# Optimization experiments

Hardware: AMD Instinct MI355X
Metric: run time of the kernel (lower is better)

Reference implementation:

```python
import jax, jax.numpy as jnp
import numpy as np
import jax.lax as lax

B, S, E, H = 8, 4096, 1024, 128
TAU = 1.0
MIN_K = 32

def setup_inputs() -> dict:
    key = jax.random.key(0)
    k0, k1, k2, k3 = jax.random.split(key, 4)
    token_embeddings = jax.random.normal(k0, (B, S, E), dtype=jnp.float32)
    w1 = jax.random.normal(k1, (E, H), dtype=jnp.float32) * (1.0 / np.sqrt(E))
    b1 = jnp.zeros((H,), dtype=jnp.float32)
    w2 = jax.random.normal(k2, (H, 1), dtype=jnp.float32) * (1.0 / np.sqrt(H))
    b2 = jnp.zeros((1,), dtype=jnp.float32)
    # uniform noise for Gumbel, same bounds as the original module
    u = jax.random.uniform(k3, (B, S), minval=1e-08, maxval=1.0 - 1e-08, dtype=jnp.float32)
    return {"token_embeddings": token_embeddings, "w1": w1, "b1": b1, "w2": w2, "b2": b2, "u": u}

def reference(token_embeddings, w1, b1, w2, b2, u):
    # scorer MLP: Dense(H) -> relu -> Dense(1), squeeze -> [B, S]
    h = jax.nn.relu(jnp.einsum('bse,eh->bsh', token_embeddings, w1) + b1)
    importance_logits = (jnp.einsum('bsh,ho->bso', h, w2) + b2)[..., 0]  # [B, S]

    # expected_k (value_function is None): soft count of kept tokens
    expected_k = jax.nn.sigmoid(importance_logits).sum(axis=-1)  # [B]
    k = jnp.clip(expected_k.astype(jnp.int32), MIN_K, None)      # [B]

    # Gumbel-softmax top-k, hard=True
    gumbel = -jnp.log(-jnp.log(u))
    soft_mask = jax.nn.softmax((importance_logits + gumbel) / TAU, axis=-1)  # [B, S]

    # hard mask: 1.0 at the top-k[i] positions of soft_mask per row.
    # Equivalent to the original argsort + while_loop scatter: positions with
    # descending-sort rank < k[i] get 1.0.
    order = jnp.argsort(-soft_mask, axis=-1)          # [B, S] descending order
    ranks = jnp.argsort(order, axis=-1)               # rank of each position
    hard_mask = (ranks < k[:, None]).astype(soft_mask.dtype)

    selection_mask = lax.stop_gradient(hard_mask - soft_mask) + soft_mask
    filtered_embeddings = token_embeddings * selection_mask[..., None]
    return filtered_embeddings, selection_mask, expected_k
```

## Files before the change

### kernel.cpp

```cpp
#include <hip/hip_runtime.h>
#include <hip/hip_bf16.h>
#include <math.h>

#define B_ 8
#define S_ 4096
#define E_ 1024
#define H_ 128
#define MIN_K 32
#define OUT_MASK_OFF (B_*S_*E_)
#define OUT_EK_OFF   (B_*S_*E_ + B_*S_)

#define LOGITS_OFF 0
#define SOFT_OFF   131072
#define CNT_OFF    262144
#define KROW_OFF   393216
#define W1T_HI_OFF 393248
#define W1T_LO_OFF 655392

typedef __attribute__((ext_vector_type(8))) short   frag8;
typedef __attribute__((ext_vector_type(4))) float   fragc;
typedef __attribute__((ext_vector_type(4))) unsigned short us4;

static __device__ __forceinline__ unsigned short bf16_rne(float f) {
  unsigned u = __float_as_uint(f);
  unsigned r = u + 0x7FFF + ((u >> 16) & 1);
  return (unsigned short)(r >> 16);
}
static __device__ __forceinline__ float bf16_to_f32(unsigned short h) {
  return __uint_as_float(((unsigned)h) << 16);
}

__global__ __launch_bounds__(256) void prep_w_kernel(
    const float* __restrict__ w1,
    unsigned short* __restrict__ w1t_hi, unsigned short* __restrict__ w1t_lo)
{
  int id = blockIdx.x * 256 + threadIdx.x;
  int k  = id >> 5;
  int n4 = id & 31;
  float4 w = *(const float4*)(w1 + k * H_ + n4 * 4);
#pragma unroll
  for (int e = 0; e < 4; ++e) {
    float f = (e == 0) ? w.x : (e == 1) ? w.y : (e == 2) ? w.z : w.w;
    unsigned short hi = bf16_rne(f);
    unsigned short lo = bf16_rne(f - bf16_to_f32(hi));
    int n = n4 * 4 + e;
    w1t_hi[n * E_ + k] = hi;
    w1t_lo[n * E_ + k] = lo;
  }
}

#define KT 32
#define XS_STRIDE 40

__global__ __launch_bounds__(256) void scorer_kernel(
    const float* __restrict__ x,
    const unsigned short* __restrict__ w1t_hi,
    const unsigned short* __restrict__ w1t_lo,
    const float* __restrict__ b1, const float* __restrict__ w2,
    const float* __restrict__ b2, float* __restrict__ logits)
{
  __shared__ unsigned short xs_hi[64 * XS_STRIDE];
  __shared__ unsigned short xs_lo[64 * XS_STRIDE];
  __shared__ float part[4][64];

  const int tid  = threadIdx.x;
  const int wave = tid >> 6;
  const int lane = tid & 63;
  const int l15  = lane & 15;
  const int quad = lane >> 4;
  const int m0   = blockIdx.x * 64;
  const int nbase = wave * 32;

  fragc acc[4][2];
#pragma unroll
  for (int mt = 0; mt < 4; ++mt)
#pragma unroll
    for (int nt = 0; nt < 2; ++nt)
      acc[mt][nt] = (fragc)(0.f);

  const int sm0 = tid >> 3, skq0 = tid & 7;
  const int sm1 = (tid + 256) >> 3, skq1 = (tid + 256) & 7;

  float4 p0 = *(const float4*)(x + (size_t)(m0 + sm0) * E_ + skq0 * 4);
  float4 p1 = *(const float4*)(x + (size_t)(m0 + sm1) * E_ + skq1 * 4);

  for (int k0 = 0; k0 < E_; k0 += KT) {
    __syncthreads();
    {
      us4 h4, l4;
      float fv[4] = {p0.x, p0.y, p0.z, p0.w};
#pragma unroll
      for (int e = 0; e < 4; ++e) {
        unsigned short hi = bf16_rne(fv[e]);
        h4[e] = hi; l4[e] = bf16_rne(fv[e] - bf16_to_f32(hi));
      }
      *(us4*)&xs_hi[sm0 * XS_STRIDE + skq0 * 4] = h4;
      *(us4*)&xs_lo[sm0 * XS_STRIDE + skq0 * 4] = l4;
      float gv[4] = {p1.x, p1.y, p1.z, p1.w};
#pragma unroll
      for (int e = 0; e < 4; ++e) {
        unsigned short hi = bf16_rne(gv[e]);
        h4[e] = hi; l4[e] = bf16_rne(gv[e] - bf16_to_f32(hi));
      }
      *(us4*)&xs_hi[sm1 * XS_STRIDE + skq1 * 4] = h4;
      *(us4*)&xs_lo[sm1 * XS_STRIDE + skq1 * 4] = l4;
    }
    __syncthreads();

    if (k0 + KT < E_) {
      p0 = *(const float4*)(x + (size_t)(m0 + sm0) * E_ + (k0 + KT) + skq0 * 4);
      p1 = *(const float4*)(x + (size_t)(m0 + sm1) * E_ + (k0 + KT) + skq1 * 4);
    }

    frag8 ah[4], al[4];
#pragma unroll
    for (int mt = 0; mt < 4; ++mt) {
      int a = (mt * 16 + l15) * XS_STRIDE + quad * 8;
      ah[mt] = *(const frag8*)&xs_hi[a];
      al[mt] = *(const frag8*)&xs_lo[a];
    }
    frag8 bh[2], bl[2];
#pragma unroll
    for (int nt = 0; nt < 2; ++nt) {
      int n = nbase + nt * 16 + l15;
      size_t off = (size_t)n * E_ + k0 + quad * 8;
      bh[nt] = *(const frag8*)(w1t_hi + off);
      bl[nt] = *(const frag8*)(w1t_lo + off);
    }
#pragma unroll
    for (int mt = 0; mt < 4; ++mt)
#pragma unroll
      for (int nt = 0; nt < 2; ++nt) {
        acc[mt][nt] = __builtin_amdgcn_mfma_f32_16x16x32_bf16(ah[mt], bh[nt], acc[mt][nt], 0, 0, 0);
        acc[mt][nt] = __builtin_amdgcn_mfma_f32_16x16x32_bf16(ah[mt], bl[nt], acc[mt][nt], 0, 0, 0);
        acc[mt][nt] = __builtin_amdgcn_mfma_f32_16x16x32_bf16(al[mt], bh[nt], acc[mt][nt], 0, 0, 0);
      }
  }

  float b1v[2], w2v[2];
#pragma unroll
  for (int nt = 0; nt < 2; ++nt) {
    int n = nbase + nt * 16 + l15;
    b1v[nt] = b1[n]; w2v[nt] = w2[n];
  }
  float v[4][4];
#pragma unroll
  for (int mt = 0; mt < 4; ++mt)
#pragma unroll
    for (int reg = 0; reg < 4; ++reg) {
      float p = 0.f;
#pragma unroll
      for (int nt = 0; nt < 2; ++nt) {
        float h = acc[mt][nt][reg] + b1v[nt];
        h = h > 0.f ? h : 0.f;
        p = fmaf(h, w2v[nt], p);
      }
      v[mt][reg] = p;
    }
#pragma unroll
  for (int mask = 1; mask < 16; mask <<= 1)
#pragma unroll
    for (int mt = 0; mt < 4; ++mt)
#pragma unroll
      for (int reg = 0; reg < 4; ++reg)
        v[mt][reg] += __shfl_xor(v[mt][reg], mask);

  if (l15 == 0) {
#pragma unroll
    for (int mt = 0; mt < 4; ++mt)
#pragma unroll
      for (int reg = 0; reg < 4; ++reg)
        part[wave][mt * 16 + quad * 4 + reg] = v[mt][reg];
  }
  __syncthreads();
  if (tid < 64)
    logits[m0 + tid] = ((part[0][tid] + part[1][tid]) + (part[2][tid] + part[3][tid])) + b2[0];
}

__global__ __launch_bounds__(1024) void row_kernel(
    const float* __restrict__ logits, const float* __restrict__ u,
    float* __restrict__ soft, int* __restrict__ krow, float* __restrict__ ek_out)
{
  const int b = blockIdx.x;
  const int t = threadIdx.x;
  const float* Lrow = logits + b * S_;
  const float* urow = u + b * S_;

  __shared__ double red[1024];
  __shared__ float  redf[1024];

  float z[4];
  double psig = 0.0;
  float zmax = -INFINITY;
#pragma unroll
  for (int i = 0; i < 4; ++i) {
    int j = t + i * 1024;
    float L = Lrow[j];
    float g = -logf(-logf(urow[j]));
    z[i] = L + g;
    psig += (double)(1.f / (1.f + expf(-L)));
    zmax = fmaxf(zmax, z[i]);
  }
  red[t] = psig; redf[t] = zmax;
  __syncthreads();
  for (int s2 = 512; s2 > 0; s2 >>= 1) {
    if (t < s2) { red[t] += red[t + s2]; redf[t] = fmaxf(redf[t], redf[t + s2]); }
    __syncthreads();
  }
  __shared__ float m_sh; __shared__ double ek_sh;
  if (t == 0) { m_sh = redf[0]; ek_sh = red[0]; }
  __syncthreads();
  float m = m_sh;

  float e[4];
  double pexp = 0.0;
#pragma unroll
  for (int i = 0; i < 4; ++i) { e[i] = expf(z[i] - m); pexp += (double)e[i]; }
  red[t] = pexp;
  __syncthreads();
  for (int s2 = 512; s2 > 0; s2 >>= 1) {
    if (t < s2) red[t] += red[t + s2];
    __syncthreads();
  }
  __shared__ float den_sh;
  if (t == 0) den_sh = (float)red[0];
  __syncthreads();
  float den = den_sh;
#pragma unroll
  for (int i = 0; i < 4; ++i) soft[b * S_ + t + i * 1024] = e[i] / den;

  if (t == 0) {
    float ekf = (float)ek_sh;
    int k = (int)ekf;
    if (k < MIN_K) k = MIN_K;
    krow[b] = k;
    ek_out[b] = ekf;
  }
}

__global__ __launch_bounds__(256) void rank_kernel(
    const float* __restrict__ soft, int* __restrict__ counts)
{
  __shared__ float4 sjs[256];
  const int b  = blockIdx.z;
  const int ic = blockIdx.x;
  const int jc = blockIdx.y;
  const int tid = threadIdx.x;
  const float* row = soft + b * S_;

  sjs[tid] = ((const float4*)row)[jc * 256 + tid];
  const int i = ic * 256 + tid;
  const float si = row[i];
  __syncthreads();

  int cnt = 0;
  const int jbase = jc * 1024;
  for (int j4 = 0; j4 < 256; ++j4) {
    float4 vv = sjs[j4];
    int j = jbase + j4 * 4;
    cnt += (vv.x > si) || (vv.x == si && (j + 0) < i);
    cnt += (vv.y > si) || (vv.y == si && (j + 1) < i);
    cnt += (vv.z > si) || (vv.z == si && (j + 2) < i);
    cnt += (vv.w > si) || (vv.w == si && (j + 3) < i);
  }
  atomicAdd(&counts[b * S_ + i], cnt);
}

__global__ __launch_bounds__(256) void filter_kernel(
    const float* __restrict__ x, const float* __restrict__ soft,
    const int* __restrict__ counts, const int* __restrict__ krow,
    float* __restrict__ out, float* __restrict__ mask_out)
{
  const int token = blockIdx.x;
  const int b = token >> 12;
  const float s = soft[token];
  const float h = (counts[token] < krow[b]) ? 1.f : 0.f;
  const float sel = (h - s) + s;

  size_t base = (size_t)token * (E_ / 4) + threadIdx.x;
  float4 v = ((const float4*)x)[base];
  v.x *= sel; v.y *= sel; v.z *= sel; v.w *= sel;
  ((float4*)out)[base] = v;
  if (threadIdx.x == 0) mask_out[token] = sel;
}

extern "C" void kernel_launch(void* const* d_in, const int* in_sizes, int n_in,
                              void* d_out, int out_size, void* d_ws, size_t ws_size,
                              hipStream_t stream) {
  const float* x  = (const float*)d_in[0];
  const float* w1 = (const float*)d_in[1];
  const float* b1 = (const float*)d_in[2];
  const float* w2 = (const float*)d_in[3];
  const float* b2 = (const float*)d_in[4];
  const float* u  = (const float*)d_in[5];

  float* out = (float*)d_out;
  float* out_filt = out;
  float* out_mask = out + OUT_MASK_OFF;
  float* out_ek   = out + OUT_EK_OFF;

  char* ws = (char*)d_ws;
  float*          ws_logits = (float*)(ws + LOGITS_OFF);
  float*          ws_soft   = (float*)(ws + SOFT_OFF);
  int*            ws_cnt    = (int*)(ws + CNT_OFF);
  int*            ws_krow   = (int*)(ws + KROW_OFF);
  unsigned short* ws_w1thi  = (unsigned short*)(ws + W1T_HI_OFF);
  unsigned short* ws_w1tlo  = (unsigned short*)(ws + W1T_LO_OFF);

  hipMemsetAsync(ws_cnt, 0, B_ * S_ * sizeof(int), stream);
  prep_w_kernel<<<dim3(128), dim3(256), 0, stream>>>(w1, ws_w1thi, ws_w1tlo);
  scorer_kernel<<<dim3(B_ * S_ / 64), dim3(256), 0, stream>>>(
      x, ws_w1thi, ws_w1tlo, b1, w2, b2, ws_logits);
  row_kernel<<<dim3(B_), dim3(1024), 0, stream>>>(ws_logits, u, ws_soft, ws_krow, out_ek);
  rank_kernel<<<dim3(16, 4, 8), dim3(256), 0, stream>>>(ws_soft, ws_cnt);
  filter_kernel<<<dim3(B_ * S_), dim3(256), 0, stream>>>(
      x, ws_soft, ws_cnt, ws_krow, out_filt, out_mask);
}
```

Baseline: 320.1 us.

## Double-buffer scorer LDS tiles, prefetch weights, and halve rows per block

The scorer kernel now handles 32 rows per block instead of 64, doubling the grid to 1024 blocks. It double-buffers the bf16 hi/lo LDS tiles so only one barrier is needed per K step, prefetches x two tiles ahead, and prefetches the next W1 fragments into registers. The goal is to hide global-load latency and raise occupancy (launch bounds 256,4) for this memory-bound GEMV-like pass over x. In exchange, each W1 fragment is reused across only two M tiles instead of four, so weight loads per FLOP double.

```diff
diff --git a/kernel.cpp b/kernel.cpp
--- a/kernel.cpp
+++ b/kernel.cpp
@@ -51,90 +51,95 @@
 
 #define KT 32
 #define XS_STRIDE 40
-
-__global__ __launch_bounds__(256) void scorer_kernel(
+#define NTILES (E_ / KT)
+
+__global__ __launch_bounds__(256, 4) void scorer_kernel(
     const float* __restrict__ x,
     const unsigned short* __restrict__ w1t_hi,
     const unsigned short* __restrict__ w1t_lo,
     const float* __restrict__ b1, const float* __restrict__ w2,
     const float* __restrict__ b2, float* __restrict__ logits)
 {
-  __shared__ unsigned short xs_hi[64 * XS_STRIDE];
-  __shared__ unsigned short xs_lo[64 * XS_STRIDE];
-  __shared__ float part[4][64];
+  __shared__ unsigned short xs_hi[2][32 * XS_STRIDE];
+  __shared__ unsigned short xs_lo[2][32 * XS_STRIDE];
+  __shared__ float part[4][32];
 
   const int tid  = threadIdx.x;
   const int wave = tid >> 6;
   const int lane = tid & 63;
   const int l15  = lane & 15;
   const int quad = lane >> 4;
-  const int m0   = blockIdx.x * 64;
+  const int m0   = blockIdx.x * 32;
   const int nbase = wave * 32;
 
-  fragc acc[4][2];
-#pragma unroll
-  for (int mt = 0; mt < 4; ++mt)
+  fragc acc[2][2];
+#pragma unroll
+  for (int mt = 0; mt < 2; ++mt)
 #pragma unroll
     for (int nt = 0; nt < 2; ++nt)
       acc[mt][nt] = (fragc)(0.f);
 
-  const int sm0 = tid >> 3, skq0 = tid & 7;
-  const int sm1 = (tid + 256) >> 3, skq1 = (tid + 256) & 7;
-
-  float4 p0 = *(const float4*)(x + (size_t)(m0 + sm0) * E_ + skq0 * 4);
-  float4 p1 = *(const float4*)(x + (size_t)(m0 + sm1) * E_ + skq1 * 4);
-
-  for (int k0 = 0; k0 < E_; k0 += KT) {
-    __syncthreads();
+  const int sm = tid >> 3, skq = tid & 7;
+  const float* xrow = x + (size_t)(m0 + sm) * E_ + skq * 4;
+
+  float4 pa = *(const float4*)(xrow);
+  float4 pb = *(const float4*)(xrow + KT);
+
+  frag8 bh[2], bl[2], bhn[2], bln[2];
+#pragma unroll
+  for (int nt = 0; nt < 2; ++nt) {
+    int n = nbase + nt * 16 + l15;
+    size_t off = (size_t)n * E_ + quad * 8;
+    bh[nt] = *(const frag8*)(w1t_hi + off);
+    bl[nt] = *(const frag8*)(w1t_lo + off);
+  }
+
+#pragma unroll 2
+  for (int t = 0; t < NTILES; ++t) {
+    const int buf = t & 1;
     {
       us4 h4, l4;
-      float fv[4] = {p0.x, p0.y, p0.z, p0.w};
+      float fv[4] = {pa.x, pa.y, pa.z, pa.w};
 #pragma unroll
       for (int e = 0; e < 4; ++e) {
         unsigned short hi = bf16_rne(fv[e]);
         h4[e] = hi; l4[e] = bf16_rne(fv[e] - bf16_to_f32(hi));
       }
-      *(us4*)&xs_hi[sm0 * XS_STRIDE + skq0 * 4] = h4;
-      *(us4*)&xs_lo[sm0 * XS_STRIDE + skq0 * 4] = l4;
-      float gv[4] = {p1.x, p1.y, p1.z, p1.w};
-#pragma unroll
-      for (int e = 0; e < 4; ++e) {
-        unsigned short hi = bf16_rne(gv[e]);
-        h4[e] = hi; l4[e] = bf16_rne(gv[e] - bf16_to_f32(hi));
-      }
-      *(us4*)&xs_hi[sm1 * XS_STRIDE + skq1 * 4] = h4;
-      *(us4*)&xs_lo[sm1 * XS_STRIDE + skq1 * 4] = l4;
+      *(us4*)&xs_hi[buf][sm * XS_STRIDE + skq * 4] = h4;
+      *(us4*)&xs_lo[buf][sm * XS_STRIDE + skq * 4] = l4;
     }
     __syncthreads();
 
-    if (k0 + KT < E_) {
-      p0 = *(const float4*)(x + (size_t)(m0 + sm0) * E_ + (k0 + KT) + skq0 * 4);
-      p1 = *(const float4*)(x + (size_t)(m0 + sm1) * E_ + (k0 + KT) + skq1 * 4);
+    pa = pb;
+    if (t + 2 < NTILES)
+      pb = *(const float4*)(xrow + (t + 2) * KT);
+    if (t + 1 < NTILES) {
+#pragma unroll
+      for (int nt = 0; nt < 2; ++nt) {
+        int n = nbase + nt * 16 + l15;
+        size_t off = (size_t)n * E_ + (t + 1) * KT + quad * 8;
+        bhn[nt] = *(const frag8*)(w1t_hi + off);
+        bln[nt] = *(const frag8*)(w1t_lo + off);
+      }
     }
 
-    frag8 ah[4], al[4];
-#pragma unroll
-    for (int mt = 0; mt < 4; ++mt) {
+    frag8 ah[2], al[2];
+#pragma unroll
+    for (int mt = 0; mt < 2; ++mt) {
       int a = (mt * 16 + l15) * XS_STRIDE + quad * 8;
-      ah[mt] = *(const frag8*)&xs_hi[a];
-      al[mt] = *(const frag8*)&xs_lo[a];
+      ah[mt] = *(const frag8*)&xs_hi[buf][a];
+      al[mt] = *(const frag8*)&xs_lo[buf][a];
     }
-    frag8 bh[2], bl[2];
-#pragma unroll
-    for (int nt = 0; nt < 2; ++nt) {
-      int n = nbase + nt * 16 + l15;
-      size_t off = (size_t)n * E_ + k0 + quad * 8;
-      bh[nt] = *(const frag8*)(w1t_hi + off);
-      bl[nt] = *(const frag8*)(w1t_lo + off);
-    }
-#pragma unroll
-    for (int mt = 0; mt < 4; ++mt)
+#pragma unroll
+    for (int mt = 0; mt < 2; ++mt)
 #pragma unroll
       for (int nt = 0; nt < 2; ++nt) {
         acc[mt][nt] = __builtin_amdgcn_mfma_f32_16x16x32_bf16(ah[mt], bh[nt], acc[mt][nt], 0, 0, 0);
         acc[mt][nt] = __builtin_amdgcn_mfma_f32_16x16x32_bf16(ah[mt], bl[nt], acc[mt][nt], 0, 0, 0);
         acc[mt][nt] = __builtin_amdgcn_mfma_f32_16x16x32_bf16(al[mt], bh[nt], acc[mt][nt], 0, 0, 0);
       }
+#pragma unroll
+    for (int nt = 0; nt < 2; ++nt) { bh[nt] = bhn[nt]; bl[nt] = bln[nt]; }
   }
 
   float b1v[2], w2v[2];
@@ -143,9 +148,9 @@
     int n = nbase + nt * 16 + l15;
     b1v[nt] = b1[n]; w2v[nt] = w2[n];
   }
-  float v[4][4];
-#pragma unroll
-  for (int mt = 0; mt < 4; ++mt)
+  float v[2][4];
+#pragma unroll
+  for (int mt = 0; mt < 2; ++mt)
 #pragma unroll
     for (int reg = 0; reg < 4; ++reg) {
       float p = 0.f;
@@ -160,20 +165,20 @@
 #pragma unroll
   for (int mask = 1; mask < 16; mask <<= 1)
 #pragma unroll
-    for (int mt = 0; mt < 4; ++mt)
+    for (int mt = 0; mt < 2; ++mt)
 #pragma unroll
       for (int reg = 0; reg < 4; ++reg)
         v[mt][reg] += __shfl_xor(v[mt][reg], mask);
 
   if (l15 == 0) {
 #pragma unroll
-    for (int mt = 0; mt < 4; ++mt)
+    for (int mt = 0; mt < 2; ++mt)
 #pragma unroll
       for (int reg = 0; reg < 4; ++reg)
         part[wave][mt * 16 + quad * 4 + reg] = v[mt][reg];
   }
   __syncthreads();
-  if (tid < 64)
+  if (tid < 32)
     logits[m0 + tid] = ((part[0][tid] + part[1][tid]) + (part[2][tid] + part[3][tid])) + b2[0];
 }
 
@@ -309,7 +314,7 @@
 
   hipMemsetAsync(ws_cnt, 0, B_ * S_ * sizeof(int), stream);
   prep_w_kernel<<<dim3(128), dim3(256), 0, stream>>>(w1, ws_w1thi, ws_w1tlo);
-  scorer_kernel<<<dim3(B_ * S_ / 64), dim3(256), 0, stream>>>(
+  scorer_kernel<<<dim3(B_ * S_ / 32), dim3(256), 0, stream>>>(
       x, ws_w1thi, ws_w1tlo, b1, w2, b2, ws_logits);
   row_kernel<<<dim3(B_), dim3(1024), 0, stream>>>(ws_logits, u, ws_soft, ws_krow, out_ek);
   rank_kernel<<<dim3(16, 4, 8), dim3(256), 0, stream>>>(ws_soft, ws_cnt);
```

Result: slower. 351.4 us (+9.8%).
